# Kernel optimization log

Hardware: AMD Instinct MI355X
Metric: run time of the kernel (lower is better)

Reference implementation:

```python
import jax, jax.numpy as jnp
import numpy as np

N = 50000        # nodes
E = 1600000      # edges (before self loops)
IN_DIM = 300     # input feature size
HID = 256        # hidden size
HEADS = 8
OC = HID // HEADS  # out channels per head = 32
LAYERS = 4
B = 1024         # number of target pairs
C = 3            # num classes
NEG_SLOPE = 0.2  # PyG GATConv leaky_relu slope


def setup_inputs() -> dict:
    key = jax.random.key(0)
    ks = jax.random.split(key, 12)

    def glorot(k, shape):
        lim = np.sqrt(6.0 / (shape[-2] + shape[-1]))
        return jax.random.uniform(k, shape, jnp.float32, -lim, lim)

    return {
        "x": jax.random.normal(ks[0], (N, IN_DIM), jnp.float32),
        "edge_index": jax.random.randint(ks[1], (2, E), 0, N, jnp.int64 if jax.config.jax_enable_x64 else jnp.int32),
        "target_mask": jax.random.randint(ks[2], (B, 2), 0, N, jnp.int64 if jax.config.jax_enable_x64 else jnp.int32),
        # lin1: [IN_DIM, HID] (stored pre-transposed vs torch)
        "lin1_W": glorot(ks[3], (IN_DIM, HID)),
        "lin1_b": jnp.zeros((HID,), jnp.float32),
        # stacked GATConv params
        "convs_W": glorot(ks[4], (LAYERS, HID, HEADS * OC)),
        "convs_att_dst": glorot(ks[5], (LAYERS, HEADS, OC)),  # att half applied to x_i (target)
        "convs_att_src": glorot(ks[6], (LAYERS, HEADS, OC)),  # att half applied to x_j (source)
        "convs_b": jnp.zeros((LAYERS, HID), jnp.float32),
        # lin3: [2*HID, C]
        "lin3_W": glorot(ks[7], (2 * HID, C)),
        "lin3_b": jnp.zeros((C,), jnp.float32),
    }


def gat_layer(h, src, tgt, W, att_dst, att_src, bias):
    """PyG-style GATConv (concat heads), edge list already includes self loops.
    h: [N, HID]; src/tgt: [E+N]; W: [HID, HEADS*OC]."""
    hw = (h @ W).reshape(N, HEADS, OC)
    # per-node attention scores, gathered per-edge (avoids materializing concat features)
    s_dst = jnp.einsum("nho,ho->nh", hw, att_dst)  # score for target role
    s_src = jnp.einsum("nho,ho->nh", hw, att_src)  # score for source role
    alpha = jax.nn.leaky_relu(s_dst[tgt] + s_src[src], NEG_SLOPE)  # [Etot, HEADS]
    # softmax over edges sharing the same target node (self loops => no empty segments)
    m = jax.ops.segment_max(alpha, tgt, num_segments=N)
    ex = jnp.exp(alpha - m[tgt])
    denom = jax.ops.segment_sum(ex, tgt, num_segments=N)
    a = ex / (denom[tgt] + 1e-16)
    # weighted scatter-aggregate of source features
    out = jax.ops.segment_sum(hw[src] * a[:, :, None], tgt, num_segments=N)  # [N, HEADS, OC]
    return out.reshape(N, HEADS * OC) + bias


def reference(x, edge_index, target_mask, lin1_W, lin1_b, convs_W,
              convs_att_dst, convs_att_src, convs_b, lin3_W, lin3_b):
    # add self loops once (PyG GATConv does this per layer; same edge set every layer)
    loop = jnp.arange(N, dtype=edge_index.dtype)
    src = jnp.concatenate([edge_index[0], loop])
    tgt = jnp.concatenate([edge_index[1], loop])

    h = x @ lin1_W + lin1_b
    for l in range(LAYERS):
        h = jax.nn.elu(gat_layer(h, src, tgt, convs_W[l],
                                 convs_att_dst[l], convs_att_src[l], convs_b[l]))
    # gather the two target nodes per sample and flatten -> [B, 2*HID]
    feats = h[target_mask].reshape(B, 2 * HID)
    logits = feats @ lin3_W + lin3_b
    return logits
```

## Files before the change

kernel.cpp:

```cpp
#include <hip/hip_runtime.h>
#include <math.h>

#define N_NODES 50000
#define N_PAD   50048
#define E_EDGES 1600000
#define ETOT    (E_EDGES + N_NODES)
#define EPAD    (E_EDGES + 8 * N_NODES)
#define IN_DIM  300
#define KP1     320
#define HID     256
#define HEADS   8
#define OC      32
#define LAYERS  4
#define BSAMP   1024
#define NEG_SLOPE 0.2f

#define NB     8
#define NPB    6250
#define BCAP   262144
#define NBLK_P 512
#define NBLK_S 196
#define NBLK_B 2048
#define NAGG   2048

typedef unsigned long long ull;
typedef unsigned short u16;
typedef _Float16 half8 __attribute__((ext_vector_type(8)));
typedef _Float16 half4v __attribute__((ext_vector_type(4)));
typedef float f32x4 __attribute__((ext_vector_type(4)));

#define GLDS16(g, l) __builtin_amdgcn_global_load_lds( \
    (const __attribute__((address_space(1))) void*)(g), \
    (__attribute__((address_space(3))) void*)(l), 16, 0, 0)


__global__ __launch_bounds__(256) void part_count_kernel(const int* __restrict__ tgt,
                                                         int* __restrict__ gcount) {
    __shared__ int cnt[NB];
    if (threadIdx.x < NB) cnt[threadIdx.x] = 0;
    __syncthreads();
    const int chunk = (ETOT + NBLK_P - 1) / NBLK_P;
    int beg = blockIdx.x * chunk;
    int end = min(beg + chunk, ETOT);
    for (int e = beg + threadIdx.x; e < end; e += 256) {
        int t_ = (e < E_EDGES) ? tgt[e] : (e - E_EDGES);
        atomicAdd(&cnt[t_ / NPB], 1);
    }
    __syncthreads();
    if (threadIdx.x < NB) gcount[blockIdx.x * NB + threadIdx.x] = cnt[threadIdx.x];
}

__global__ __launch_bounds__(512) void part_scan_kernel(const int* __restrict__ gcount,
                                                        int* __restrict__ goff,
                                                        int* __restrict__ bcnt) {
    __shared__ int arr[NBLK_P][NB];
    int k = threadIdx.x;
    int4 a = ((const int4*)gcount)[k * 2];
    int4 b = ((const int4*)gcount)[k * 2 + 1];
    int own[NB] = {a.x, a.y, a.z, a.w, b.x, b.y, b.z, b.w};
    #pragma unroll
    for (int j = 0; j < NB; j++) arr[k][j] = own[j];
    __syncthreads();
    for (int off = 1; off < NBLK_P; off <<= 1) {
        int tmp[NB];
        #pragma unroll
        for (int j = 0; j < NB; j++) tmp[j] = (k >= off) ? arr[k - off][j] : 0;
        __syncthreads();
        #pragma unroll
        for (int j = 0; j < NB; j++) arr[k][j] += tmp[j];
        __syncthreads();
    }
    int ex[NB];
    #pragma unroll
    for (int j = 0; j < NB; j++) ex[j] = arr[k][j] - own[j];
    ((int4*)goff)[k * 2]     = make_int4(ex[0], ex[1], ex[2], ex[3]);
    ((int4*)goff)[k * 2 + 1] = make_int4(ex[4], ex[5], ex[6], ex[7]);
    if (k == NBLK_P - 1) {
        #pragma unroll
        for (int j = 0; j < NB; j++) bcnt[j] = arr[k][j];
    }
}

__global__ __launch_bounds__(256) void part_scatter_kernel(const int* __restrict__ src,
                                                           const int* __restrict__ tgt,
                                                           const int* __restrict__ goff,
                                                           ull* __restrict__ bpart) {
    __shared__ int cur[NB];
    if (threadIdx.x < NB) cur[threadIdx.x] = goff[blockIdx.x * NB + threadIdx.x];
    __syncthreads();
    const int chunk = (ETOT + NBLK_P - 1) / NBLK_P;
    int beg = blockIdx.x * chunk;
    int end = min(beg + chunk, ETOT);
    for (int e = beg + threadIdx.x; e < end; e += 256) {
        int s_, t_;
        if (e < E_EDGES) { s_ = src[e]; t_ = tgt[e]; }
        else             { s_ = t_ = e - E_EDGES; }
        int b = t_ / NPB;
        int pos = atomicAdd(&cur[b], 1);
        bpart[(size_t)b * BCAP + pos] = ((ull)(unsigned)t_ << 32) | (unsigned)s_;
    }
}

__global__ __launch_bounds__(256) void count_edges_kernel(const ull* __restrict__ bpart,
                                                          const int* __restrict__ bcnt,
                                                          int* counts) {
    int b = blockIdx.x & (NB - 1);
    int ib = blockIdx.x >> 3;
    int nblk = gridDim.x >> 3;
    int nb = bcnt[b];
    const ull* bp = bpart + (size_t)b * BCAP;
    for (int i = ib * 256 + threadIdx.x; i < nb; i += nblk * 256)
        atomicAdd(&counts[(int)(bp[i] >> 32)], 1);
}

__global__ __launch_bounds__(256) void scan1_kernel(const int* __restrict__ counts,
                                                    int* __restrict__ row_ptr,
                                                    int* __restrict__ bsum) {
    __shared__ int sums[256];
    int t = threadIdx.x;
    int i = blockIdx.x * 256 + t;
    int c = (i < N_NODES) ? ((counts[i] + 7) & ~7) : 0;
    sums[t] = c;
    __syncthreads();
    for (int off = 1; off < 256; off <<= 1) {
        int a = sums[t];
        int u = (t >= off) ? sums[t - off] : 0;
        __syncthreads();
        sums[t] = a + u;
        __syncthreads();
    }
    if (i < N_NODES) row_ptr[i] = sums[t] - c;
    if (t == 255) bsum[blockIdx.x] = sums[255];
}

__global__ __launch_bounds__(256) void scan2_kernel(const int* __restrict__ bsum,
                                                    int* __restrict__ boff,
                                                    int* __restrict__ row_ptr) {
    __shared__ int sums[256];
    int t = threadIdx.x;
    int b = (t < NBLK_S) ? bsum[t] : 0;
    sums[t] = b;
    __syncthreads();
    for (int off = 1; off < 256; off <<= 1) {
        int a = sums[t];
        int u = (t >= off) ? sums[t - off] : 0;
        __syncthreads();
        sums[t] = a + u;
        __syncthreads();
    }
    if (t < NBLK_S) boff[t] = sums[t] - b;
    if (t == 255) row_ptr[N_NODES] = sums[255];
}

__global__ __launch_bounds__(256) void scan3_kernel(int* __restrict__ row_ptr,
                                                    const int* __restrict__ boff,
                                                    int* __restrict__ cursor) {
    int i = blockIdx.x * 256 + threadIdx.x;
    if (i >= N_NODES) return;
    int v = row_ptr[i] + boff[blockIdx.x];
    row_ptr[i] = v;
    cursor[i]  = v;
}

__global__ __launch_bounds__(256) void fill_edges_kernel(const ull* __restrict__ bpart,
                                                         const int* __restrict__ bcnt,
                                                         int* cursor, u16* __restrict__ col) {
    int b = blockIdx.x & (NB - 1);
    int ib = blockIdx.x >> 3;
    int nblk = gridDim.x >> 3;
    int nb = bcnt[b];
    const ull* bp = bpart + (size_t)b * BCAP;
    for (int i = ib * 256 + threadIdx.x; i < nb; i += nblk * 256) {
        ull pk = bp[i];
        int t_ = (int)(pk >> 32);
        int s_ = (int)pk;
        int pos = atomicAdd(&cursor[t_], 1);
        col[pos] = (u16)s_;
    }
}

__global__ __launch_bounds__(256) void pad_edges_kernel(const int* __restrict__ cursor,
                                                        const int* __restrict__ row_ptr,
                                                        u16* __restrict__ col) {
    int i = blockIdx.x * 256 + threadIdx.x;
    if (i >= N_NODES) return;
    int e = cursor[i];
    int pe = row_ptr[i + 1];
    for (; e < pe; e++) col[e] = (u16)i;
}


__global__ __launch_bounds__(256) void cast_x_kernel(const float* __restrict__ x, _Float16* __restrict__ xh) {
    int i = blockIdx.x * 256 + threadIdx.x;
    if (i >= N_NODES * (KP1 / 8)) return;
    int r = i / (KP1 / 8), c8 = i % (KP1 / 8);
    half8 o;
    const float4* xr = (const float4*)(x + (size_t)r * IN_DIM);
    if (c8 < 37) {
        float4 u = xr[c8 * 2], v = xr[c8 * 2 + 1];
        o[0] = (_Float16)u.x; o[1] = (_Float16)u.y; o[2] = (_Float16)u.z; o[3] = (_Float16)u.w;
        o[4] = (_Float16)v.x; o[5] = (_Float16)v.y; o[6] = (_Float16)v.z; o[7] = (_Float16)v.w;
    } else if (c8 == 37) {
        float4 u = xr[74];
        o[0] = (_Float16)u.x; o[1] = (_Float16)u.y; o[2] = (_Float16)u.z; o[3] = (_Float16)u.w;
        o[4] = o[5] = o[6] = o[7] = (_Float16)0.f;
    } else {
        #pragma unroll
        for (int j = 0; j < 8; j++) o[j] = (_Float16)0.f;
    }
    ((half8*)xh)[i] = o;
}

__global__ __launch_bounds__(256) void cast_w1_kernel(const float* __restrict__ W, _Float16* __restrict__ Wt) {
    int i = blockIdx.x * 256 + threadIdx.x;
    if (i >= HID * KP1) return;
    int n = i / KP1, k = i % KP1;
    float v = (k < IN_DIM) ? W[(size_t)k * HID + n] : 0.f;
    Wt[i] = (_Float16)v;
}

__global__ __launch_bounds__(256) void cast_wc_kernel(const float* __restrict__ W, _Float16* __restrict__ Wt) {
    int i = blockIdx.x * 256 + threadIdx.x;
    if (i >= LAYERS * HID * HID) return;
    int l = i / (HID * HID);
    int r = i % (HID * HID);
    int n = r / HID, k = r % HID;
    Wt[i] = (_Float16)W[(size_t)l * HID * HID + (size_t)k * HID + n];
}

__global__ __launch_bounds__(256) void gemm_mfma_kernel(const _Float16* __restrict__ A,
                                                        const _Float16* __restrict__ Wt,
                                                        const float* __restrict__ bias,
                                                        _Float16* __restrict__ C,
                                                        int M, int Kp, int addbias,
                                                        int headmajor) {
    __shared__ _Float16 As[128][32];
    __shared__ _Float16 Bs[128][32];
    const int tid = threadIdx.x;
    const int m0 = blockIdx.x * 128;
    const int n0 = blockIdx.y * 128;
    const int w = tid >> 6, lane = tid & 63;
    const int wm = (w & 1) * 64, wn = (w >> 1) * 64;
    const int quad = lane >> 4, m16 = lane & 15;

    f32x4 acc[4][4];
    #pragma unroll
    for (int i = 0; i < 4; i++)
        #pragma unroll
        for (int j = 0; j < 4; j++)
            acc[i][j] = (f32x4){0.f, 0.f, 0.f, 0.f};

    char* lA = (char*)&As[0][0] + w * 1024;
    char* lB = (char*)&Bs[0][0] + w * 1024;

    for (int k0 = 0; k0 < Kp; k0 += 32) {
        #pragma unroll
        for (int i = 0; i < 2; i++) {
            int seg = tid + i * 256;
            int row = seg >> 2, off = seg & 3;
            GLDS16(&A[(size_t)(m0 + row) * Kp + k0 + off * 8], lA + i * 4096);
            GLDS16(&Wt[(size_t)(n0 + row) * Kp + k0 + off * 8], lB + i * 4096);
        }
        __syncthreads();

        half8 af[4], bf[4];
        #pragma unroll
        for (int i = 0; i < 4; i++) {
            af[i] = *(const half8*)&As[wm + i * 16 + m16][quad * 8];
            bf[i] = *(const half8*)&Bs[wn + i * 16 + m16][quad * 8];
        }
        #pragma unroll
        for (int mi = 0; mi < 4; mi++)
            #pragma unroll
            for (int ni = 0; ni < 4; ni++)
                acc[mi][ni] = __builtin_amdgcn_mfma_f32_16x16x32_f16(af[mi], bf[ni], acc[mi][ni], 0, 0, 0);
        __syncthreads();
    }

    #pragma unroll
    for (int mi = 0; mi < 4; mi++) {
        #pragma unroll
        for (int r = 0; r < 4; r++) {
            int row = m0 + wm + mi * 16 + quad * 4 + r;
            if (row < M) {
                #pragma unroll
                for (int ni = 0; ni < 4; ni++) {
                    int colg = n0 + wn + ni * 16 + m16;
                    float v = acc[mi][ni][r];
                    if (addbias) v += bias[colg];
                    if (headmajor) {
                        int hd = colg >> 5, oc = colg & 31;
                        C[((size_t)hd * N_NODES + row) * 32 + oc] = (_Float16)v;
                    } else {
                        C[(size_t)row * HID + colg] = (_Float16)v;
                    }
                }
            }
        }
    }
}

__global__ __launch_bounds__(256) void score_kernel(const _Float16* __restrict__ hw,
                                                    const float* __restrict__ att_dst,
                                                    const float* __restrict__ att_src,
                                                    float* __restrict__ s_dst,
                                                    float* __restrict__ s_src) {
    int wv = threadIdx.x >> 6, lane = threadIdx.x & 63;
    int nd = lane >> 3, hd = lane & 7;
    float4 ad[8], as4[8];
    const float4* A4d = (const float4*)att_dst;
    const float4* A4s = (const float4*)att_src;
    #pragma unroll
    for (int j = 0; j < 8; j++) { ad[j] = A4d[hd * 8 + j]; as4[j] = A4s[hd * 8 + j]; }
    const half8* hw8 = (const half8*)hw;
    int nwaves = gridDim.x * 4;
    for (int g = blockIdx.x * 4 + wv; g < N_NODES / 8; g += nwaves) {
        int node = g * 8 + nd;
        float sd = 0.f, ss = 0.f;
        #pragma unroll
        for (int k = 0; k < 4; k++) {
            half8 v = hw8[((size_t)hd * N_NODES + node) * 4 + k];
            #pragma unroll
            for (int i = 0; i < 8; i++) {
                float f = (float)v[i];
                int q = k * 8 + i;
                sd += f * ((const float*)&ad[q >> 2])[q & 3];
                ss += f * ((const float*)&as4[q >> 2])[q & 3];
            }
        }
        s_dst[(size_t)hd * N_NODES + node] = sd;
        s_src[(size_t)hd * N_NODES + node] = ss;
    }
}

__global__ __launch_bounds__(256, 8) void agg_kernel(const int* __restrict__ row_ptr,
                                                     const int* __restrict__ deg_arr,
                                                     const u16* __restrict__ col,
                                                     const float* __restrict__ s_dst,
                                                     const float* __restrict__ s_src,
                                                     const _Float16* __restrict__ hw,
                                                     const float* __restrict__ bias,
                                                     _Float16* __restrict__ h_out) {
    __shared__ float exL[4][128];
    __shared__ int   snL[4][128];

    const int wv   = threadIdx.x >> 6;
    const int lane = threadIdx.x & 63;
    const int head = blockIdx.x & (NB - 1);
    const int ib   = blockIdx.x >> 3;
    const int es   = lane >> 3;
    const int cl   = lane & 7;
    const int wid  = ib * 4 + wv;
    const int NW   = (NAGG / NB) * 4;

    const float* sdh = s_dst + (size_t)head * N_NODES;
    const float* ssh = s_src + (size_t)head * N_NODES;
    const char*  hwb = (const char*)(hw + (size_t)head * N_NODES * 32) + cl * 8;

    const float* bpt = bias + head * 32 + cl * 4;
    float b0 = bpt[0], b1 = bpt[1], b2 = bpt[2], b3 = bpt[3];

    float* exw = &exL[wv][0];
    int*   snw = &snL[wv][0];

    for (int t = wid; t < N_NODES; t += NW) {
        int start = row_ptr[t];
        int pdeg  = row_ptr[t + 1] - start;
        int deg   = deg_arr[t];
        float sdv = sdh[t];
        const u16* cb = col + start;

        float dsumL = 0.f;
        float a0 = 0.f, a1 = 0.f, a2 = 0.f, a3 = 0.f;

        for (int c0 = 0; c0 < pdeg; c0 += 128) {
            int csz = min(pdeg - c0, 128);

            for (int b = 0; b < csz; b += 64) {
                int slot = b + lane;
                bool act = slot < csz;
                int sn = 0;
                if (act) sn = (int)cb[c0 + slot];
                float ss = ssh[(unsigned)sn];
                float a = sdv + ss;
                a = (a > 0.f) ? a : NEG_SLOPE * a;
                float ex = (act && (c0 + slot) < deg) ? __expf(a) : 0.f;
                if (act) { exw[slot] = ex; snw[slot] = sn << 6; }
                dsumL += ex;
            }

            int ngrp = csz >> 3;
            int d0 = snw[es];
            int d1 = (ngrp > 1) ? snw[8 + es] : 0;
            half4v v0 = *(const half4v*)(hwb + (unsigned)d0);
            for (int g = 0; g < ngrp; g++) {
                int d2 = (g + 2 < ngrp) ? snw[(g + 2) * 8 + es] : 0;
                half4v vn = *(const half4v*)(hwb + (unsigned)d1);
                float e = exw[g * 8 + es];
                a0 += e * (float)v0[0];
                a1 += e * (float)v0[1];
                a2 += e * (float)v0[2];
                a3 += e * (float)v0[3];
                v0 = vn; d1 = d2;
            }
        }

        #pragma unroll
        for (int off = 1; off <= 32; off <<= 1) dsumL += __shfl_xor(dsumL, off);
        #pragma unroll
        for (int off = 8; off <= 32; off <<= 1) {
            a0 += __shfl_xor(a0, off);
            a1 += __shfl_xor(a1, off);
            a2 += __shfl_xor(a2, off);
            a3 += __shfl_xor(a3, off);
        }

        if (es == 0) {
            float inv = 1.f / (dsumL + 1e-16f);
            float o0 = a0 * inv + b0;
            float o1 = a1 * inv + b1;
            float o2 = a2 * inv + b2;
            float o3 = a3 * inv + b3;
            o0 = (o0 > 0.f) ? o0 : (__expf(o0) - 1.f);
            o1 = (o1 > 0.f) ? o1 : (__expf(o1) - 1.f);
            o2 = (o2 > 0.f) ? o2 : (__expf(o2) - 1.f);
            o3 = (o3 > 0.f) ? o3 : (__expf(o3) - 1.f);
            half4v ov;
            ov[0] = (_Float16)o0; ov[1] = (_Float16)o1;
            ov[2] = (_Float16)o2; ov[3] = (_Float16)o3;
            *(half4v*)(h_out + (size_t)t * HID + head * 32 + cl * 4) = ov;
        }
    }
}

__global__ __launch_bounds__(256) void head_kernel(const _Float16* __restrict__ h,
                                                   const int* __restrict__ target_mask,
                                                   const float* __restrict__ W,
                                                   const float* __restrict__ b,
                                                   float* __restrict__ out) {
    int s = blockIdx.x;
    int t = threadIdx.x;
    int n0 = target_mask[s * 2 + 0];
    int n1 = target_mask[s * 2 + 1];
    float f0 = (float)h[(size_t)n0 * HID + t];
    float f1 = (float)h[(size_t)n1 * HID + t];
    float a0 = f0 * W[t * 3 + 0] + f1 * W[(t + 256) * 3 + 0];
    float a1 = f0 * W[t * 3 + 1] + f1 * W[(t + 256) * 3 + 1];
    float a2 = f0 * W[t * 3 + 2] + f1 * W[(t + 256) * 3 + 2];
    #pragma unroll
    for (int off = 32; off >= 1; off >>= 1) {
        a0 += __shfl_xor(a0, off);
        a1 += __shfl_xor(a1, off);
        a2 += __shfl_xor(a2, off);
    }
    __shared__ float red[4][3];
    int wv = t >> 6, ln = t & 63;
    if (ln == 0) { red[wv][0] = a0; red[wv][1] = a1; red[wv][2] = a2; }
    __syncthreads();
    if (t < 3) {
        out[s * 3 + t] = red[0][t] + red[1][t] + red[2][t] + red[3][t] + b[t];
    }
}


extern "C" void kernel_launch(void* const* d_in, const int* in_sizes, int n_in,
                              void* d_out, int out_size, void* d_ws, size_t ws_size,
                              hipStream_t stream) {
    const float* x        = (const float*)d_in[0];
    const int*   eidx     = (const int*)  d_in[1];
    const int*   tmask    = (const int*)  d_in[2];
    const float* lin1_W   = (const float*)d_in[3];
    const float* lin1_b   = (const float*)d_in[4];
    const float* convs_W  = (const float*)d_in[5];
    const float* att_dst  = (const float*)d_in[6];
    const float* att_src  = (const float*)d_in[7];
    const float* convs_b  = (const float*)d_in[8];
    const float* lin3_W   = (const float*)d_in[9];
    const float* lin3_b   = (const float*)d_in[10];
    float* out = (float*)d_out;

    char* ws = (char*)d_ws;
    size_t off = 0;
    auto alloc = [&](size_t bytes) -> void* {
        void* p = ws + off;
        off = (off + bytes + 255) & ~(size_t)255;
        return p;
    };
    _Float16* xh   = (_Float16*)alloc((size_t)N_PAD * KP1 * 2);
    _Float16* h    = (_Float16*)alloc((size_t)N_PAD * HID * 2);
    _Float16* hw   = (_Float16*)alloc((size_t)N_PAD * HID * 2);
    _Float16* w1t  = (_Float16*)alloc((size_t)HID * KP1 * 2);
    _Float16* wct  = (_Float16*)alloc((size_t)LAYERS * HID * HID * 2);
    float* sdst    = (float*)alloc((size_t)HEADS * N_NODES * 4);
    float* ssrc    = (float*)alloc((size_t)HEADS * N_NODES * 4);
    int*   counts  = (int*)  alloc((size_t)N_NODES * 4);
    int*   rowptr  = (int*)  alloc((size_t)(N_NODES + 1) * 4);
    int*   cursor  = (int*)  alloc((size_t)N_NODES * 4);
    u16*   col     = (u16*)  alloc((size_t)(EPAD + 32) * 2);
    ull*   bpart   = (ull*)  alloc((size_t)NB * BCAP * 8);
    int*   bcnt    = (int*)  alloc((size_t)NB * 4);
    int*   gcount  = (int*)  alloc((size_t)NBLK_P * NB * 4);
    int*   goff    = (int*)  alloc((size_t)NBLK_P * NB * 4);
    int*   bsum    = (int*)  alloc((size_t)NBLK_S * 4);
    int*   boff    = (int*)  alloc((size_t)NBLK_S * 4);

    const int* src = eidx;
    const int* tgt = eidx + E_EDGES;

    hipMemsetAsync(counts, 0, (size_t)N_NODES * 4, stream);
    part_count_kernel<<<NBLK_P, 256, 0, stream>>>(tgt, gcount);
    part_scan_kernel<<<1, NBLK_P, 0, stream>>>(gcount, goff, bcnt);
    part_scatter_kernel<<<NBLK_P, 256, 0, stream>>>(src, tgt, goff, bpart);
    count_edges_kernel<<<NBLK_B, 256, 0, stream>>>(bpart, bcnt, counts);
    scan1_kernel<<<NBLK_S, 256, 0, stream>>>(counts, rowptr, bsum);
    scan2_kernel<<<1, 256, 0, stream>>>(bsum, boff, rowptr);
    scan3_kernel<<<NBLK_S, 256, 0, stream>>>(rowptr, boff, cursor);
    fill_edges_kernel<<<NBLK_B, 256, 0, stream>>>(bpart, bcnt, cursor, col);
    pad_edges_kernel<<<(N_NODES + 255) / 256, 256, 0, stream>>>(cursor, rowptr, col);

    cast_x_kernel<<<(N_NODES * (KP1 / 8) + 255) / 256, 256, 0, stream>>>(x, xh);
    cast_w1_kernel<<<(HID * KP1 + 255) / 256, 256, 0, stream>>>(lin1_W, w1t);
    cast_wc_kernel<<<(LAYERS * HID * HID + 255) / 256, 256, 0, stream>>>(convs_W, wct);

    gemm_mfma_kernel<<<dim3((N_NODES + 127) / 128, HID / 128), 256, 0, stream>>>(
        xh, w1t, lin1_b, h, N_NODES, KP1, 1, 0);

    for (int l = 0; l < LAYERS; l++) {
        gemm_mfma_kernel<<<dim3((N_NODES + 127) / 128, HID / 128), 256, 0, stream>>>(
            h, wct + (size_t)l * HID * HID, nullptr, hw, N_NODES, HID, 0, 1);
        score_kernel<<<256, 256, 0, stream>>>(
            hw, att_dst + (size_t)l * HEADS * OC, att_src + (size_t)l * HEADS * OC, sdst, ssrc);
        agg_kernel<<<NAGG, 256, 0, stream>>>(
            rowptr, counts, col, sdst, ssrc, hw, convs_b + (size_t)l * HID, h);
    }

    head_kernel<<<BSAMP, 256, 0, stream>>>(h, tmask, lin3_W, lin3_b, out);
}
```

Measured before the change: 1.124 ms.

## Process two target nodes per wave in GAT aggregation and drop degree masking

Each wave in the aggregation kernel now handles two consecutive target nodes. It stages both nodes' attention weights and source indices into separate shared-memory buffers before gathering features, so independent memory work overlaps. Padding edges now point to a sentinel node whose source score is -1e30, so their exp weight is zero. This removes the per-edge degree check, the deg array argument, and a separate full-wave denominator reduction. The sentinel reads a feature row past the head's node range, which for the last head lands in uninitialised padding. If that memory holds NaN or Inf, multiplying by a zero weight can still corrupt results.

```diff
diff --git a/kernel.cpp b/kernel.cpp
--- a/kernel.cpp
+++ b/kernel.cpp
@@ -14,6 +14,7 @@
 #define LAYERS  4
 #define BSAMP   1024
 #define NEG_SLOPE 0.2f
+#define NS1     (N_NODES + 1)
 
 #define NB     8
 #define NPB    6250
@@ -186,7 +187,7 @@
     if (i >= N_NODES) return;
     int e = cursor[i];
     int pe = row_ptr[i + 1];
-    for (; e < pe; e++) col[e] = (u16)i;
+    for (; e < pe; e++) col[e] = (u16)N_NODES;
 }
 
 
@@ -305,6 +306,8 @@
                                                     const float* __restrict__ att_src,
                                                     float* __restrict__ s_dst,
                                                     float* __restrict__ s_src) {
+    if (blockIdx.x == 0 && threadIdx.x < HEADS)
+        s_src[(size_t)threadIdx.x * NS1 + N_NODES] = -1e30f;
     int wv = threadIdx.x >> 6, lane = threadIdx.x & 63;
     int nd = lane >> 3, hd = lane & 7;
     float4 ad[8], as4[8];
@@ -329,20 +332,19 @@
             }
         }
         s_dst[(size_t)hd * N_NODES + node] = sd;
-        s_src[(size_t)hd * N_NODES + node] = ss;
+        s_src[(size_t)hd * NS1 + node] = ss;
     }
 }
 
 __global__ __launch_bounds__(256, 8) void agg_kernel(const int* __restrict__ row_ptr,
-                                                     const int* __restrict__ deg_arr,
                                                      const u16* __restrict__ col,
                                                      const float* __restrict__ s_dst,
                                                      const float* __restrict__ s_src,
                                                      const _Float16* __restrict__ hw,
                                                      const float* __restrict__ bias,
                                                      _Float16* __restrict__ h_out) {
-    __shared__ float exL[4][128];
-    __shared__ int   snL[4][128];
+    __shared__ float exL[4][2][128];
+    __shared__ int   snL[4][2][128];
 
     const int wv   = threadIdx.x >> 6;
     const int lane = threadIdx.x & 63;
@@ -354,73 +356,105 @@
     const int NW   = (NAGG / NB) * 4;
 
     const float* sdh = s_dst + (size_t)head * N_NODES;
-    const float* ssh = s_src + (size_t)head * N_NODES;
-    const char*  hwb = (const char*)(hw + (size_t)head * N_NODES * 32) + cl * 8;
+    const float* ssh = s_src + (size_t)head * NS1;
+    const char*  hwh = (const char*)(hw + (size_t)head * N_NODES * 32);
+    const unsigned vcl = (unsigned)(cl * 8);
 
     const float* bpt = bias + head * 32 + cl * 4;
     float b0 = bpt[0], b1 = bpt[1], b2 = bpt[2], b3 = bpt[3];
 
-    float* exw = &exL[wv][0];
-    int*   snw = &snL[wv][0];
-
-    for (int t = wid; t < N_NODES; t += NW) {
-        int start = row_ptr[t];
-        int pdeg  = row_ptr[t + 1] - start;
-        int deg   = deg_arr[t];
-        float sdv = sdh[t];
-        const u16* cb = col + start;
-
-        float dsumL = 0.f;
-        float a0 = 0.f, a1 = 0.f, a2 = 0.f, a3 = 0.f;
-
-        for (int c0 = 0; c0 < pdeg; c0 += 128) {
-            int csz = min(pdeg - c0, 128);
-
-            for (int b = 0; b < csz; b += 64) {
-                int slot = b + lane;
-                bool act = slot < csz;
-                int sn = 0;
-                if (act) sn = (int)cb[c0 + slot];
+    auto stageA = [&](int s, int start, int pdeg, float sdv) {
+        float* exw = &exL[wv][s][0];
+        int*   snw = &snL[wv][s][0];
+        for (int b = 0; b < pdeg; b += 64) {
+            int slot = b + lane;
+            if (slot < pdeg) {
+                int sn = (int)col[start + slot];
                 float ss = ssh[(unsigned)sn];
                 float a = sdv + ss;
-                a = (a > 0.f) ? a : NEG_SLOPE * a;
-                float ex = (act && (c0 + slot) < deg) ? __expf(a) : 0.f;
-                if (act) { exw[slot] = ex; snw[slot] = sn << 6; }
-                dsumL += ex;
+                a = fmaxf(a, NEG_SLOPE * a);
+                exw[slot] = __expf(a);
+                snw[slot] = sn << 6;
             }
-
-            int ngrp = csz >> 3;
-            int d0 = snw[es];
-            int d1 = (ngrp > 1) ? snw[8 + es] : 0;
-            half4v v0 = *(const half4v*)(hwb + (unsigned)d0);
-            for (int g = 0; g < ngrp; g++) {
-                int d2 = (g + 2 < ngrp) ? snw[(g + 2) * 8 + es] : 0;
-                half4v vn = *(const half4v*)(hwb + (unsigned)d1);
-                float e = exw[g * 8 + es];
-                a0 += e * (float)v0[0];
-                a1 += e * (float)v0[1];
-                a2 += e * (float)v0[2];
-                a3 += e * (float)v0[3];
-                v0 = vn; d1 = d2;
+        }
+    };
+
+    auto phaseC = [&](int s, int pdeg, float& dsum,
+                      float& a0, float& a1, float& a2, float& a3) {
+        float* exw = &exL[wv][s][0];
+        int*   snw = &snL[wv][s][0];
+        int ngrp = pdeg >> 3;
+        int d0 = snw[es];
+        int d1 = (ngrp > 1) ? snw[8 + es] : d0;
+        half4v v0 = *(const half4v*)(hwh + ((unsigned)d0 | vcl));
+        for (int g = 0; g < ngrp; g++) {
+            int d2 = (g + 2 < ngrp) ? snw[(g + 2) * 8 + es] : 0;
+            half4v vn = *(const half4v*)(hwh + ((unsigned)d1 | vcl));
+            float e = exw[g * 8 + es];
+            dsum += e;
+            a0 += e * (float)v0[0];
+            a1 += e * (float)v0[1];
+            a2 += e * (float)v0[2];
+            a3 += e * (float)v0[3];
+            v0 = vn; d1 = d2;
+        }
+    };
+
+    for (int tb = wid * 2; tb < N_NODES; tb += NW * 2) {
+        int t0 = tb, t1 = tb + 1;
+        int r0 = row_ptr[t0];
+        int r1 = row_ptr[t1];
+        int r2 = row_ptr[t1 + 1];
+        int pd0 = r1 - r0, pd1 = r2 - r1;
+        float sdv0 = sdh[t0], sdv1 = sdh[t1];
+
+        float ds0 = 0.f, ds1 = 0.f;
+        float x0 = 0.f, x1 = 0.f, x2 = 0.f, x3 = 0.f;
+        float y0 = 0.f, y1 = 0.f, y2 = 0.f, y3 = 0.f;
+
+        if (pd0 <= 128 && pd1 <= 128) {
+            stageA(0, r0, pd0, sdv0);
+            stageA(1, r1, pd1, sdv1);
+            phaseC(0, pd0, ds0, x0, x1, x2, x3);
+            phaseC(1, pd1, ds1, y0, y1, y2, y3);
+        } else {
+            for (int c0 = 0; c0 < pd0; c0 += 128) {
+                int csz = min(pd0 - c0, 128);
+                stageA(0, r0 + c0, csz, sdv0);
+                phaseC(0, csz, ds0, x0, x1, x2, x3);
             }
-        }
-
-        #pragma unroll
-        for (int off = 1; off <= 32; off <<= 1) dsumL += __shfl_xor(dsumL, off);
+            for (int c0 = 0; c0 < pd1; c0 += 128) {
+                int csz = min(pd1 - c0, 128);
+                stageA(1, r1 + c0, csz, sdv1);
+                phaseC(1, csz, ds1, y0, y1, y2, y3);
+            }
+        }
+
         #pragma unroll
         for (int off = 8; off <= 32; off <<= 1) {
-            a0 += __shfl_xor(a0, off);
-            a1 += __shfl_xor(a1, off);
-            a2 += __shfl_xor(a2, off);
-            a3 += __shfl_xor(a3, off);
-        }
-
-        if (es == 0) {
-            float inv = 1.f / (dsumL + 1e-16f);
-            float o0 = a0 * inv + b0;
-            float o1 = a1 * inv + b1;
-            float o2 = a2 * inv + b2;
-            float o3 = a3 * inv + b3;
+            ds0 += __shfl_xor(ds0, off);
+            ds1 += __shfl_xor(ds1, off);
+            x0 += __shfl_xor(x0, off);
+            x1 += __shfl_xor(x1, off);
+            x2 += __shfl_xor(x2, off);
+            x3 += __shfl_xor(x3, off);
+            y0 += __shfl_xor(y0, off);
+            y1 += __shfl_xor(y1, off);
+            y2 += __shfl_xor(y2, off);
+            y3 += __shfl_xor(y3, off);
+        }
+
+        if (es < 2) {
+            float ds = (es == 0) ? ds0 : ds1;
+            float s0 = (es == 0) ? x0 : y0;
+            float s1 = (es == 0) ? x1 : y1;
+            float s2 = (es == 0) ? x2 : y2;
+            float s3 = (es == 0) ? x3 : y3;
+            float inv = 1.f / (ds + 1e-16f);
+            float o0 = s0 * inv + b0;
+            float o1 = s1 * inv + b1;
+            float o2 = s2 * inv + b2;
+            float o3 = s3 * inv + b3;
             o0 = (o0 > 0.f) ? o0 : (__expf(o0) - 1.f);
             o1 = (o1 > 0.f) ? o1 : (__expf(o1) - 1.f);
             o2 = (o2 > 0.f) ? o2 : (__expf(o2) - 1.f);
@@ -428,7 +462,7 @@
             half4v ov;
             ov[0] = (_Float16)o0; ov[1] = (_Float16)o1;
             ov[2] = (_Float16)o2; ov[3] = (_Float16)o3;
-            *(half4v*)(h_out + (size_t)t * HID + head * 32 + cl * 4) = ov;
+            *(half4v*)(h_out + (size_t)(tb + es) * HID + head * 32 + cl * 4) = ov;
         }
     }
 }
@@ -492,7 +526,7 @@
     _Float16* w1t  = (_Float16*)alloc((size_t)HID * KP1 * 2);
     _Float16* wct  = (_Float16*)alloc((size_t)LAYERS * HID * HID * 2);
     float* sdst    = (float*)alloc((size_t)HEADS * N_NODES * 4);
-    float* ssrc    = (float*)alloc((size_t)HEADS * N_NODES * 4);
+    float* ssrc    = (float*)alloc((size_t)HEADS * NS1 * 4);
     int*   counts  = (int*)  alloc((size_t)N_NODES * 4);
     int*   rowptr  = (int*)  alloc((size_t)(N_NODES + 1) * 4);
     int*   cursor  = (int*)  alloc((size_t)N_NODES * 4);
@@ -531,7 +565,7 @@
         score_kernel<<<256, 256, 0, stream>>>(
             hw, att_dst + (size_t)l * HEADS * OC, att_src + (size_t)l * HEADS * OC, sdst, ssrc);
         agg_kernel<<<NAGG, 256, 0, stream>>>(
-            rowptr, counts, col, sdst, ssrc, hw, convs_b + (size_t)l * HID, h);
+            rowptr, col, sdst, ssrc, hw, convs_b + (size_t)l * HID, h);
     }
 
     head_kernel<<<BSAMP, 256, 0, stream>>>(h, tmask, lin3_W, lin3_b, out);
```

Measured after the change: 1.024 ms. 1.1x faster.

## Process two target nodes per wave in GAT aggregation with sentinel padding

Applied to the files above, without the earlier changes.

The aggregation kernel now has each wavefront handle two destination nodes at once. Each half-wave gathers 8 fp16 channels per lane (16-byte loads) instead of 4. Padding edges point at a sentinel node whose source score is -1e30, so their exp is zero and the per-edge degree check and deg array are no longer needed. The denominator is accumulated inside the gather loop. The goal is fewer idle lanes on low-degree nodes and wider memory transactions. The cost is a separate slow path for high-degree nodes, extra LDS zero-filling, and a larger score grid.

```diff
diff --git a/kernel.cpp b/kernel.cpp
--- a/kernel.cpp
+++ b/kernel.cpp
@@ -14,6 +14,7 @@
 #define LAYERS  4
 #define BSAMP   1024
 #define NEG_SLOPE 0.2f
+#define NS1     (N_NODES + 1)
 
 #define NB     8
 #define NPB    6250
@@ -186,7 +187,7 @@
     if (i >= N_NODES) return;
     int e = cursor[i];
     int pe = row_ptr[i + 1];
-    for (; e < pe; e++) col[e] = (u16)i;
+    for (; e < pe; e++) col[e] = (u16)N_NODES;
 }
 
 
@@ -305,6 +306,8 @@
                                                     const float* __restrict__ att_src,
                                                     float* __restrict__ s_dst,
                                                     float* __restrict__ s_src) {
+    if (blockIdx.x == 0 && threadIdx.x < HEADS)
+        s_src[(size_t)threadIdx.x * NS1 + N_NODES] = -1e30f;
     int wv = threadIdx.x >> 6, lane = threadIdx.x & 63;
     int nd = lane >> 3, hd = lane & 7;
     float4 ad[8], as4[8];
@@ -329,106 +332,147 @@
             }
         }
         s_dst[(size_t)hd * N_NODES + node] = sd;
-        s_src[(size_t)hd * N_NODES + node] = ss;
+        s_src[(size_t)hd * NS1 + node] = ss;
     }
 }
 
 __global__ __launch_bounds__(256, 8) void agg_kernel(const int* __restrict__ row_ptr,
-                                                     const int* __restrict__ deg_arr,
                                                      const u16* __restrict__ col,
                                                      const float* __restrict__ s_dst,
                                                      const float* __restrict__ s_src,
                                                      const _Float16* __restrict__ hw,
                                                      const float* __restrict__ bias,
                                                      _Float16* __restrict__ h_out) {
-    __shared__ float exL[4][128];
-    __shared__ int   snL[4][128];
+    __shared__ float exL[4][2][128];
+    __shared__ int   snL[4][2][128];
 
     const int wv   = threadIdx.x >> 6;
     const int lane = threadIdx.x & 63;
     const int head = blockIdx.x & (NB - 1);
     const int ib   = blockIdx.x >> 3;
-    const int es   = lane >> 3;
-    const int cl   = lane & 7;
+    const int nh   = lane >> 5;
+    const int es   = (lane >> 2) & 7;
+    const int cl   = lane & 3;
     const int wid  = ib * 4 + wv;
     const int NW   = (NAGG / NB) * 4;
 
     const float* sdh = s_dst + (size_t)head * N_NODES;
-    const float* ssh = s_src + (size_t)head * N_NODES;
-    const char*  hwb = (const char*)(hw + (size_t)head * N_NODES * 32) + cl * 8;
-
-    const float* bpt = bias + head * 32 + cl * 4;
-    float b0 = bpt[0], b1 = bpt[1], b2 = bpt[2], b3 = bpt[3];
-
-    float* exw = &exL[wv][0];
-    int*   snw = &snL[wv][0];
-
-    for (int t = wid; t < N_NODES; t += NW) {
-        int start = row_ptr[t];
-        int pdeg  = row_ptr[t + 1] - start;
-        int deg   = deg_arr[t];
-        float sdv = sdh[t];
-        const u16* cb = col + start;
-
-        float dsumL = 0.f;
-        float a0 = 0.f, a1 = 0.f, a2 = 0.f, a3 = 0.f;
-
-        for (int c0 = 0; c0 < pdeg; c0 += 128) {
-            int csz = min(pdeg - c0, 128);
-
-            for (int b = 0; b < csz; b += 64) {
-                int slot = b + lane;
-                bool act = slot < csz;
-                int sn = 0;
-                if (act) sn = (int)cb[c0 + slot];
-                float ss = ssh[(unsigned)sn];
-                float a = sdv + ss;
-                a = (a > 0.f) ? a : NEG_SLOPE * a;
-                float ex = (act && (c0 + slot) < deg) ? __expf(a) : 0.f;
-                if (act) { exw[slot] = ex; snw[slot] = sn << 6; }
-                dsumL += ex;
-            }
-
-            int ngrp = csz >> 3;
-            int d0 = snw[es];
-            int d1 = (ngrp > 1) ? snw[8 + es] : 0;
-            half4v v0 = *(const half4v*)(hwb + (unsigned)d0);
-            for (int g = 0; g < ngrp; g++) {
-                int d2 = (g + 2 < ngrp) ? snw[(g + 2) * 8 + es] : 0;
-                half4v vn = *(const half4v*)(hwb + (unsigned)d1);
-                float e = exw[g * 8 + es];
-                a0 += e * (float)v0[0];
-                a1 += e * (float)v0[1];
-                a2 += e * (float)v0[2];
-                a3 += e * (float)v0[3];
-                v0 = vn; d1 = d2;
-            }
-        }
-
-        #pragma unroll
-        for (int off = 1; off <= 32; off <<= 1) dsumL += __shfl_xor(dsumL, off);
-        #pragma unroll
-        for (int off = 8; off <= 32; off <<= 1) {
+    const float* ssh = s_src + (size_t)head * NS1;
+    const char*  hwh = (const char*)(hw + (size_t)head * N_NODES * 32);
+    const unsigned vcl = (unsigned)(cl * 16);
+
+    float bb[8];
+    {
+        const float* bpt = bias + head * 32 + cl * 8;
+        #pragma unroll
+        for (int i = 0; i < 8; i++) bb[i] = bpt[i];
+    }
+
+    float* exw = &exL[wv][nh][0];
+    int*   snw = &snL[wv][nh][0];
+
+    auto stage = [&](int s, int startg, int csz, float sdv) {
+        float* exd = &exL[wv][s][0];
+        int*   snd = &snL[wv][s][0];
+        for (int b = 0; b < csz; b += 64) {
+            int slot = b + lane;
+            if (slot < csz) {
+                int sn = (int)col[startg + slot];
+                float a = sdv + ssh[(unsigned)sn];
+                a = fmaxf(a, NEG_SLOPE * a);
+                exd[slot] = __expf(a);
+                snd[slot] = sn << 6;
+            }
+        }
+    };
+
+    float dsum, a0, a1, a2, a3, a4, a5, a6, a7;
+
+    auto phaseC = [&](int ngrp) {
+        int d0 = snw[es];
+        int d1 = (ngrp > 1) ? snw[8 + es] : 0;
+        half8 v0 = *(const half8*)(hwh + ((unsigned)d0 | vcl));
+        for (int g = 0; g < ngrp; g++) {
+            int d2 = (g + 2 < ngrp) ? snw[(g + 2) * 8 + es] : 0;
+            half8 vn = *(const half8*)(hwh + ((unsigned)d1 | vcl));
+            float e = exw[g * 8 + es];
+            dsum += e;
+            a0 += e * (float)v0[0];
+            a1 += e * (float)v0[1];
+            a2 += e * (float)v0[2];
+            a3 += e * (float)v0[3];
+            a4 += e * (float)v0[4];
+            a5 += e * (float)v0[5];
+            a6 += e * (float)v0[6];
+            a7 += e * (float)v0[7];
+            v0 = vn; d1 = d2;
+        }
+    };
+
+    for (int tb = wid * 2; tb < N_NODES; tb += NW * 2) {
+        int r0 = row_ptr[tb];
+        int r1 = row_ptr[tb + 1];
+        int r2 = row_ptr[tb + 2];
+        int pd0 = r1 - r0, pd1 = r2 - r1;
+        float sdv0 = sdh[tb], sdv1 = sdh[tb + 1];
+
+        dsum = 0.f;
+        a0 = a1 = a2 = a3 = a4 = a5 = a6 = a7 = 0.f;
+
+        if (pd0 <= 128 && pd1 <= 128) {
+            int mx = max(pd0, pd1);
+            stage(0, r0, pd0, sdv0);
+            stage(1, r1, pd1, sdv1);
+            for (int slot = pd0 + lane; slot < mx; slot += 64) {
+                exL[wv][0][slot] = 0.f; snL[wv][0][slot] = 0;
+            }
+            for (int slot = pd1 + lane; slot < mx; slot += 64) {
+                exL[wv][1][slot] = 0.f; snL[wv][1][slot] = 0;
+            }
+            phaseC(mx >> 3);
+        } else {
+            #pragma unroll 1
+            for (int s = 0; s < 2; s++) {
+                for (int slot = lane; slot < 128; slot += 64) {
+                    exL[wv][s ^ 1][slot] = 0.f; snL[wv][s ^ 1][slot] = 0;
+                }
+                int rs = s ? r1 : r0;
+                int pds = s ? pd1 : pd0;
+                float sdvs = s ? sdv1 : sdv0;
+                for (int c0 = 0; c0 < pds; c0 += 128) {
+                    int csz = min(pds - c0, 128);
+                    stage(s, rs + c0, csz, sdvs);
+                    phaseC(csz >> 3);
+                }
+            }
+        }
+
+        #pragma unroll
+        for (int off = 4; off <= 16; off <<= 1) {
+            dsum += __shfl_xor(dsum, off);
             a0 += __shfl_xor(a0, off);
             a1 += __shfl_xor(a1, off);
             a2 += __shfl_xor(a2, off);
             a3 += __shfl_xor(a3, off);
+            a4 += __shfl_xor(a4, off);
+            a5 += __shfl_xor(a5, off);
+            a6 += __shfl_xor(a6, off);
+            a7 += __shfl_xor(a7, off);
         }
 
         if (es == 0) {
-            float inv = 1.f / (dsumL + 1e-16f);
-            float o0 = a0 * inv + b0;
-            float o1 = a1 * inv + b1;
-            float o2 = a2 * inv + b2;
-            float o3 = a3 * inv + b3;
-            o0 = (o0 > 0.f) ? o0 : (__expf(o0) - 1.f);
-            o1 = (o1 > 0.f) ? o1 : (__expf(o1) - 1.f);
-            o2 = (o2 > 0.f) ? o2 : (__expf(o2) - 1.f);
-            o3 = (o3 > 0.f) ? o3 : (__expf(o3) - 1.f);
-            half4v ov;
-            ov[0] = (_Float16)o0; ov[1] = (_Float16)o1;
-            ov[2] = (_Float16)o2; ov[3] = (_Float16)o3;
-            *(half4v*)(h_out + (size_t)t * HID + head * 32 + cl * 4) = ov;
+            float inv = 1.f / (dsum + 1e-16f);
+            float o[8] = {a0 * inv + bb[0], a1 * inv + bb[1],
+                          a2 * inv + bb[2], a3 * inv + bb[3],
+                          a4 * inv + bb[4], a5 * inv + bb[5],
+                          a6 * inv + bb[6], a7 * inv + bb[7]};
+            half8 ov;
+            #pragma unroll
+            for (int i = 0; i < 8; i++) {
+                float v = (o[i] > 0.f) ? o[i] : (__expf(o[i]) - 1.f);
+                ov[i] = (_Float16)v;
+            }
+            *(half8*)(h_out + (size_t)(tb + nh) * HID + head * 32 + cl * 8) = ov;
         }
     }
 }
@@ -492,7 +536,7 @@
     _Float16* w1t  = (_Float16*)alloc((size_t)HID * KP1 * 2);
     _Float16* wct  = (_Float16*)alloc((size_t)LAYERS * HID * HID * 2);
     float* sdst    = (float*)alloc((size_t)HEADS * N_NODES * 4);
-    float* ssrc    = (float*)alloc((size_t)HEADS * N_NODES * 4);
+    float* ssrc    = (float*)alloc((size_t)HEADS * NS1 * 4);
     int*   counts  = (int*)  alloc((size_t)N_NODES * 4);
     int*   rowptr  = (int*)  alloc((size_t)(N_NODES + 1) * 4);
     int*   cursor  = (int*)  alloc((size_t)N_NODES * 4);
@@ -528,10 +572,10 @@
     for (int l = 0; l < LAYERS; l++) {
         gemm_mfma_kernel<<<dim3((N_NODES + 127) / 128, HID / 128), 256, 0, stream>>>(
             h, wct + (size_t)l * HID * HID, nullptr, hw, N_NODES, HID, 0, 1);
-        score_kernel<<<256, 256, 0, stream>>>(
+        score_kernel<<<512, 256, 0, stream>>>(
             hw, att_dst + (size_t)l * HEADS * OC, att_src + (size_t)l * HEADS * OC, sdst, ssrc);
         agg_kernel<<<NAGG, 256, 0, stream>>>(
-            rowptr, counts, col, sdst, ssrc, hw, convs_b + (size_t)l * HID, h);
+            rowptr, col, sdst, ssrc, hw, convs_b + (size_t)l * HID, h);
     }
 
     head_kernel<<<BSAMP, 256, 0, stream>>>(h, tmask, lin3_W, lin3_b, out);
```

Result: faster. 988.9 us (-12.0%).
